# Performance work log

Hardware: AMD Instinct MI355X
Metric: run time of the kernel (lower is better)

Reference implementation:

```python
import jax, jax.numpy as jnp
import numpy as np

N_NODES = 262144
N_EDGES = 524288
EMB = 256
HID = 256
NODE_VOC = 50000
POS_VOC = 1000
LN_EPS = 1e-5


def layer_norm(x, g, b):
    m = jnp.mean(x, axis=-1, keepdims=True)
    v = jnp.var(x, axis=-1, keepdims=True)
    return (x - m) * jax.lax.rsqrt(v + LN_EPS) * g + b


def sage_conv(x, src, dst, Wl, bl, Wr):
    # PyG SAGEConv, aggr='add': out = lin_l(sum_{j in N(i)} x_j) + lin_r(x_i)
    agg = jax.ops.segment_sum(x[src], dst, num_segments=N_NODES)  # [N, d_in]
    return agg @ Wl.T + bl + x @ Wr.T


def setup_inputs() -> dict:
    key = jax.random.key(0)
    ks = jax.random.split(key, 16)
    s = 0.02
    node_emb = jax.random.randint(ks[0], (N_NODES,), 0, NODE_VOC)
    pos = jax.random.randint(ks[1], (N_NODES,), 0, POS_VOC)
    edge = jax.random.randint(ks[2], (2, N_EDGES), 0, N_NODES)
    node_tab = jax.random.normal(ks[3], (NODE_VOC, EMB), jnp.float32) * s
    pos_tab = jax.random.normal(ks[4], (POS_VOC, EMB), jnp.float32) * s
    pos_tab = pos_tab.at[0].set(0.0)  # padding_idx=0
    g_emb = jnp.ones((EMB,), jnp.float32)
    b_emb = jnp.zeros((EMB,), jnp.float32)
    Wl0 = jax.random.normal(ks[5], (HID, EMB), jnp.float32) * s
    bl0 = jnp.zeros((HID,), jnp.float32)
    Wr0 = jax.random.normal(ks[6], (HID, EMB), jnp.float32) * s
    g0 = jnp.ones((HID,), jnp.float32)
    b0 = jnp.zeros((HID,), jnp.float32)
    Wl1 = jax.random.normal(ks[7], (EMB, HID), jnp.float32) * s
    bl1 = jnp.zeros((EMB,), jnp.float32)
    Wr1 = jax.random.normal(ks[8], (EMB, HID), jnp.float32) * s
    g1 = jnp.ones((EMB,), jnp.float32)
    b1 = jnp.zeros((EMB,), jnp.float32)
    return {"node_emb": node_emb, "pos": pos, "edge": edge,
            "node_tab": node_tab, "pos_tab": pos_tab,
            "g_emb": g_emb, "b_emb": b_emb,
            "Wl0": Wl0, "bl0": bl0, "Wr0": Wr0, "g0": g0, "b0": b0,
            "Wl1": Wl1, "bl1": bl1, "Wr1": Wr1, "g1": g1, "b1": b1}


def reference(node_emb, pos, edge, node_tab, pos_tab, g_emb, b_emb,
              Wl0, bl0, Wr0, g0, b0, Wl1, bl1, Wr1, g1, b1):
    src, dst = edge[0], edge[1]
    # embed + scale + positional emb; dropout is identity in eval
    h = node_tab[node_emb] * jnp.sqrt(jnp.float32(EMB)) + pos_tab[pos]
    h = layer_norm(h, g_emb, b_emb)
    for (Wl, bl, Wr, g, b) in ((Wl0, bl0, Wr0, g0, b0), (Wl1, bl1, Wr1, g1, b1)):
        h_ = jax.nn.relu(sage_conv(h, src, dst, Wl, bl, Wr))
        h = layer_norm(h_ + h, g, b)
    return h
```

## Files before the change

### kernel.cpp

```cpp
#include <hip/hip_runtime.h>
#include <hip/hip_bf16.h>
#include <stdint.h>

#define N_NODES 262144
#define N_EDGES 524288
#define EMB 256
#define LN_EPS 1e-5f

typedef unsigned short u16;
typedef unsigned int u32;
typedef __bf16 bf16_t;
typedef __bf16 bf16x8 __attribute__((ext_vector_type(8)));
typedef float f32x4 __attribute__((ext_vector_type(4)));

__device__ __forceinline__ u16 f2bf(float f) {
    u32 u = __float_as_uint(f);
    u32 r = u + 0x7fffu + ((u >> 16) & 1u);
    return (u16)(r >> 16);
}
__device__ __forceinline__ float bf2f(u16 b) { return __uint_as_float(((u32)b) << 16); }
__device__ __forceinline__ float lo16(u32 x) { return __uint_as_float(x << 16); }
__device__ __forceinline__ float hi16(u32 x) { return __uint_as_float(x & 0xffff0000u); }

__device__ __forceinline__ void async_copy16(void* lds, const void* g) {
    __builtin_amdgcn_global_load_lds(
        (const __attribute__((address_space(1))) u32*)g,
        (__attribute__((address_space(3))) u32*)lds, 16, 0, 0);
}

__global__ __launch_bounds__(256) void convert_w_kernel(
    const float* __restrict__ a, const float* __restrict__ b,
    const float* __restrict__ c, const float* __restrict__ d,
    u16* __restrict__ out)
{
    int seg = blockIdx.x >> 6;
    int blk = blockIdx.x & 63;
    const float* src = (seg == 0) ? a : (seg == 1) ? b : (seg == 2) ? c : d;
    int off = blk * 1024 + threadIdx.x * 4;
    float4 v = *(const float4*)(src + off);
    uint2 o;
    o.x = (u32)f2bf(v.x) | ((u32)f2bf(v.y) << 16);
    o.y = (u32)f2bf(v.z) | ((u32)f2bf(v.w) << 16);
    *(uint2*)(out + seg * 65536 + off) = o;
}

__global__ __launch_bounds__(256) void embed_ln_kernel(
    const int* __restrict__ node_emb, const int* __restrict__ pos,
    const float* __restrict__ node_tab, const float* __restrict__ pos_tab,
    const float* __restrict__ g_emb, const float* __restrict__ b_emb,
    u16* __restrict__ h0)
{
    const int wid = threadIdx.x >> 6, lane = threadIdx.x & 63;
    const int row = blockIdx.x * 4 + wid;
    const int idx = node_emb[row];
    const int p = pos[row];
    float4 ra = *(const float4*)(node_tab + (size_t)idx * EMB + lane * 4);
    float4 rb = *(const float4*)(pos_tab + (size_t)p * EMB + lane * 4);
    float v0 = ra.x * 16.f + rb.x;
    float v1 = ra.y * 16.f + rb.y;
    float v2 = ra.z * 16.f + rb.z;
    float v3 = ra.w * 16.f + rb.w;
    float s = v0 + v1 + v2 + v3;
    float sq = v0 * v0 + v1 * v1 + v2 * v2 + v3 * v3;
    #pragma unroll
    for (int m = 1; m < 64; m <<= 1) { s += __shfl_xor(s, m); sq += __shfl_xor(sq, m); }
    float mean = s * (1.f / 256.f);
    float var = sq * (1.f / 256.f) - mean * mean;
    float rstd = rsqrtf(var + LN_EPS);
    float4 rg = *(const float4*)(g_emb + lane * 4);
    float4 rbt = *(const float4*)(b_emb + lane * 4);
    float o0 = (v0 - mean) * rstd * rg.x + rbt.x;
    float o1 = (v1 - mean) * rstd * rg.y + rbt.y;
    float o2 = (v2 - mean) * rstd * rg.z + rbt.z;
    float o3 = (v3 - mean) * rstd * rg.w + rbt.w;
    uint2 out;
    out.x = (u32)f2bf(o0) | ((u32)f2bf(o1) << 16);
    out.y = (u32)f2bf(o2) | ((u32)f2bf(o3) << 16);
    *(uint2*)(h0 + (size_t)row * EMB + lane * 4) = out;
}

__global__ __launch_bounds__(256) void hist_kernel(const int* __restrict__ dst, int* __restrict__ deg) {
    int e = blockIdx.x * 256 + threadIdx.x;
    atomicAdd(&deg[dst[e]], 1);
}

__global__ __launch_bounds__(1024) void scan1_kernel(const int* __restrict__ deg,
                                                     int* __restrict__ incl, int* __restrict__ bsum) {
    __shared__ int tmp[1024];
    int t = threadIdx.x, g = blockIdx.x * 1024 + t;
    tmp[t] = deg[g];
    __syncthreads();
    for (int off = 1; off < 1024; off <<= 1) {
        int x = (t >= off) ? tmp[t - off] : 0;
        __syncthreads();
        tmp[t] += x;
        __syncthreads();
    }
    incl[g] = tmp[t];
    if (t == 1023) bsum[blockIdx.x] = tmp[t];
}

__global__ __launch_bounds__(256) void scan2_kernel(const int* __restrict__ bsum, int* __restrict__ boff) {
    __shared__ int tmp[256];
    int t = threadIdx.x;
    int own = bsum[t];
    tmp[t] = own;
    __syncthreads();
    for (int off = 1; off < 256; off <<= 1) {
        int x = (t >= off) ? tmp[t - off] : 0;
        __syncthreads();
        tmp[t] += x;
        __syncthreads();
    }
    boff[t] = tmp[t] - own;
}

__global__ __launch_bounds__(256) void scan3_kernel(const int* __restrict__ incl, const int* __restrict__ deg,
                                                    const int* __restrict__ boff,
                                                    int* __restrict__ rowstart, int* __restrict__ cursor) {
    int g = blockIdx.x * 256 + threadIdx.x;
    int v = incl[g] - deg[g] + boff[g >> 10];
    rowstart[g] = v;
    cursor[g] = v;
    if (g == N_NODES - 1) rowstart[N_NODES] = N_EDGES;
}

__global__ __launch_bounds__(256) void scatter_kernel(const int* __restrict__ src, const int* __restrict__ dst,
                                                      int* __restrict__ cursor, int* __restrict__ csr) {
    int e = blockIdx.x * 256 + threadIdx.x;
    int slot = atomicAdd(&cursor[dst[e]], 1);
    csr[slot] = src[e];
}

template<bool F32OUT>
__global__ __launch_bounds__(512, 4) void gemm_fused_kernel(
    const u16* __restrict__ Hin,
    const int* __restrict__ rowstart, const int* __restrict__ csr,
    const u16* __restrict__ Wl, const u16* __restrict__ Wr,
    const float* __restrict__ bias, const float* __restrict__ gam, const float* __restrict__ bet,
    u16* __restrict__ outb, float* __restrict__ outf)
{
    __shared__ alignas(16) u16 aggA[4 * 64 * 64];
    __shared__ alignas(16) u16 lB[256 * 64];
    __shared__ float s_sum[64];
    __shared__ float s_sq[64];

    const int tid = threadIdx.x;
    const int wid = tid >> 6, lane = tid & 63;
    const int quad = lane >> 4, l16 = lane & 15;
    const int wrow = wid >> 2, wcol = wid & 3;
    const int m0 = blockIdx.x * 64;
    const int lsrc = ((lane & 7) ^ (lane >> 3)) * 8;

    auto stageB = [&](int s) {
        const int k0 = s * 64;
        const u16* Bsrc = (k0 < 256) ? (Wl + k0) : (Wr + (k0 - 256));
        #pragma unroll
        for (int t = 0; t < 4; ++t) {
            int q = wid * 4 + t;
            int n = q * 8 + (lane >> 3);
            async_copy16((char*)lB + q * 1024, Bsrc + (size_t)n * EMB + lsrc);
        }
    };
    auto stageH = [&](int t) {
        int row = tid >> 3;
        int kg = (tid & 7) ^ (row & 7);
        async_copy16((char*)aggA + (t - 4) * 8192 + tid * 16,
                     Hin + (size_t)(m0 + row) * EMB + (t - 4) * 64 + kg * 8);
    };

    stageB(0);

    {
        const int grp = tid >> 5, gl = tid & 31;
        #pragma unroll
        for (int i = 0; i < 4; ++i) {
            const int r = grp * 4 + i;
            const int node = m0 + r;
            const int beg = rowstart[node];
            const int end = rowstart[node + 1];
            float a0[8] = {}, a1[8] = {};
            int j = beg;
            for (; j + 1 < end; j += 2) {
                int s0 = csr[j], s1 = csr[j + 1];
                uint4 r0 = *(const uint4*)(Hin + (size_t)s0 * EMB + gl * 8);
                uint4 r1 = *(const uint4*)(Hin + (size_t)s1 * EMB + gl * 8);
                a0[0] += lo16(r0.x); a0[1] += hi16(r0.x);
                a0[2] += lo16(r0.y); a0[3] += hi16(r0.y);
                a0[4] += lo16(r0.z); a0[5] += hi16(r0.z);
                a0[6] += lo16(r0.w); a0[7] += hi16(r0.w);
                a1[0] += lo16(r1.x); a1[1] += hi16(r1.x);
                a1[2] += lo16(r1.y); a1[3] += hi16(r1.y);
                a1[4] += lo16(r1.z); a1[5] += hi16(r1.z);
                a1[6] += lo16(r1.w); a1[7] += hi16(r1.w);
            }
            if (j < end) {
                int s0 = csr[j];
                uint4 r0 = *(const uint4*)(Hin + (size_t)s0 * EMB + gl * 8);
                a0[0] += lo16(r0.x); a0[1] += hi16(r0.x);
                a0[2] += lo16(r0.y); a0[3] += hi16(r0.y);
                a0[4] += lo16(r0.z); a0[5] += hi16(r0.z);
                a0[6] += lo16(r0.w); a0[7] += hi16(r0.w);
            }
            uint4 o;
            o.x = (u32)f2bf(a0[0] + a1[0]) | ((u32)f2bf(a0[1] + a1[1]) << 16);
            o.y = (u32)f2bf(a0[2] + a1[2]) | ((u32)f2bf(a0[3] + a1[3]) << 16);
            o.z = (u32)f2bf(a0[4] + a1[4]) | ((u32)f2bf(a0[5] + a1[5]) << 16);
            o.w = (u32)f2bf(a0[6] + a1[6]) | ((u32)f2bf(a0[7] + a1[7]) << 16);
            int cg = (gl & 7) ^ (r & 7);
            *(uint4*)&aggA[(gl >> 3) * 4096 + r * 64 + cg * 8] = o;
        }
    }
    asm volatile("s_waitcnt lgkmcnt(0)\n\ts_barrier" ::: "memory");

    f32x4 acc[2][4] = {};
    #pragma unroll
    for (int s = 0; s < 8; ++s) {
        if (s > 0) stageB(s);
        if (s >= 1 && s <= 4) stageH(s + 3);
        if (s >= 1 && s <= 4) asm volatile("s_waitcnt vmcnt(1)\n\ts_barrier" ::: "memory");
        else                  asm volatile("s_waitcnt vmcnt(0)\n\ts_barrier" ::: "memory");

        const u16* la = aggA + (s & 3) * 4096;
        #pragma unroll
        for (int kk = 0; kk < 2; ++kk) {
            const int g = (((kk * 4 + quad) ^ (l16 & 7)) * 8);
            bf16x8 af[2], bfr[4];
            #pragma unroll
            for (int mt = 0; mt < 2; ++mt)
                af[mt] = *(const bf16x8*)&la[(wrow * 32 + mt * 16 + l16) * 64 + g];
            #pragma unroll
            for (int nt = 0; nt < 4; ++nt)
                bfr[nt] = *(const bf16x8*)&lB[(wcol * 64 + nt * 16 + l16) * 64 + g];
            #pragma unroll
            for (int mt = 0; mt < 2; ++mt)
                #pragma unroll
                for (int nt = 0; nt < 4; ++nt)
                    acc[mt][nt] = __builtin_amdgcn_mfma_f32_16x16x32_bf16(af[mt], bfr[nt], acc[mt][nt], 0, 0, 0);
        }
        asm volatile("s_waitcnt lgkmcnt(0)\n\ts_barrier" ::: "memory");
    }

    if (tid < 64) { s_sum[tid] = 0.f; s_sq[tid] = 0.f; }
    __syncthreads();

    const int cb = wcol * 64;
    float blv[4], gv[4], bv[4];
    #pragma unroll
    for (int nt = 0; nt < 4; ++nt) {
        int col = cb + nt * 16 + l16;
        blv[nt] = bias[col]; gv[nt] = gam[col]; bv[nt] = bet[col];
    }

    #pragma unroll
    for (int mt = 0; mt < 2; ++mt) {
        #pragma unroll
        for (int i = 0; i < 4; ++i) {
            int r = wrow * 32 + mt * 16 + quad * 4 + i;
            int rowg = m0 + r;
            float rs = 0.f, rq = 0.f;
            #pragma unroll
            for (int nt = 0; nt < 4; ++nt) {
                int col = cb + nt * 16 + l16;
                float v = acc[mt][nt][i] + blv[nt];
                v = fmaxf(v, 0.f);
                v += bf2f(Hin[(size_t)rowg * EMB + col]);
                acc[mt][nt][i] = v;
                rs += v; rq += v * v;
            }
            #pragma unroll
            for (int m = 1; m < 16; m <<= 1) { rs += __shfl_xor(rs, m); rq += __shfl_xor(rq, m); }
            if (l16 == 0) { atomicAdd(&s_sum[r], rs); atomicAdd(&s_sq[r], rq); }
        }
    }
    __syncthreads();

    #pragma unroll
    for (int mt = 0; mt < 2; ++mt) {
        #pragma unroll
        for (int i = 0; i < 4; ++i) {
            int r = wrow * 32 + mt * 16 + quad * 4 + i;
            int rowg = m0 + r;
            float mean = s_sum[r] * (1.f / 256.f);
            float var = s_sq[r] * (1.f / 256.f) - mean * mean;
            float rstd = rsqrtf(var + LN_EPS);
            #pragma unroll
            for (int nt = 0; nt < 4; ++nt) {
                int col = cb + nt * 16 + l16;
                float o = (acc[mt][nt][i] - mean) * rstd * gv[nt] + bv[nt];
                if (F32OUT) outf[(size_t)rowg * EMB + col] = o;
                else        outb[(size_t)rowg * EMB + col] = f2bf(o);
            }
        }
    }
}

extern "C" void kernel_launch(void* const* d_in, const int* in_sizes, int n_in,
                              void* d_out, int out_size, void* d_ws, size_t ws_size,
                              hipStream_t stream)
{
    const int* node_emb = (const int*)d_in[0];
    const int* pos      = (const int*)d_in[1];
    const int* edge     = (const int*)d_in[2];
    const float* node_tab = (const float*)d_in[3];
    const float* pos_tab  = (const float*)d_in[4];
    const float* g_emb    = (const float*)d_in[5];
    const float* b_emb    = (const float*)d_in[6];
    const float* Wl0 = (const float*)d_in[7];
    const float* bl0 = (const float*)d_in[8];
    const float* Wr0 = (const float*)d_in[9];
    const float* g0  = (const float*)d_in[10];
    const float* b0  = (const float*)d_in[11];
    const float* Wl1 = (const float*)d_in[12];
    const float* bl1 = (const float*)d_in[13];
    const float* Wr1 = (const float*)d_in[14];
    const float* g1  = (const float*)d_in[15];
    const float* b1  = (const float*)d_in[16];

    char* w = (char*)d_ws;
    auto alloc = [&](size_t bytes) { char* p = w; w += (bytes + 255) & ~(size_t)255; return p; };
    u16* h0       = (u16*)alloc((size_t)N_NODES * EMB * 2);
    u16* h1       = (u16*)alloc((size_t)N_NODES * EMB * 2);
    u16* wbf      = (u16*)alloc((size_t)4 * 65536 * 2);
    int* deg      = (int*)alloc((size_t)N_NODES * 4);
    int* incl     = (int*)alloc((size_t)N_NODES * 4);
    int* rowstart = (int*)alloc((size_t)(N_NODES + 1) * 4);
    int* cursor   = (int*)alloc((size_t)N_NODES * 4);
    int* csr      = (int*)alloc((size_t)N_EDGES * 4);
    int* bsum     = (int*)alloc(256 * 4);
    int* boff     = (int*)alloc(256 * 4);

    float* outf = (float*)d_out;

    const int* srcv = edge;
    const int* dstv = edge + N_EDGES;

    hipMemsetAsync(deg, 0, (size_t)N_NODES * 4, stream);
    convert_w_kernel<<<256, 256, 0, stream>>>(Wl0, Wr0, Wl1, Wr1, wbf);
    embed_ln_kernel<<<N_NODES / 4, 256, 0, stream>>>(node_emb, pos, node_tab, pos_tab, g_emb, b_emb, h0);
    hist_kernel<<<N_EDGES / 256, 256, 0, stream>>>(dstv, deg);
    scan1_kernel<<<N_NODES / 1024, 1024, 0, stream>>>(deg, incl, bsum);
    scan2_kernel<<<1, 256, 0, stream>>>(bsum, boff);
    scan3_kernel<<<N_NODES / 256, 256, 0, stream>>>(incl, deg, boff, rowstart, cursor);
    scatter_kernel<<<N_EDGES / 256, 256, 0, stream>>>(srcv, dstv, cursor, csr);

    gemm_fused_kernel<false><<<N_NODES / 64, 512, 0, stream>>>(
        h0, rowstart, csr, wbf, wbf + 65536, bl0, g0, b0, h1, nullptr);
    gemm_fused_kernel<true><<<N_NODES / 64, 512, 0, stream>>>(
        h1, rowstart, csr, wbf + 131072, wbf + 196608, bl1, g1, b1, nullptr, outf);
}
```

Baseline: 855.7 us.

## Stage CSR indices in LDS and widen per-thread gather to 32 bytes

Before aggregation, the block's 64 rowstart entries and up to 1024 CSR neighbor indices are preloaded into shared memory, so the gather loop reads indices from LDS instead of issuing dependent global loads. Each thread now handles 16 features (two 16-byte loads per neighbor) across 2 rows instead of 8 features across 4 rows, which doubles the loads in flight per thread. The row loop is no longer unrolled. The costs are an extra barrier, about 4 KB more LDS (which may affect occupancy at launch_bounds(512,4)), and higher register pressure from 32 accumulators.

```diff
diff --git a/kernel.cpp b/kernel.cpp
--- a/kernel.cpp
+++ b/kernel.cpp
@@ -6,6 +6,7 @@
 #define N_EDGES 524288
 #define EMB 256
 #define LN_EPS 1e-5f
+#define CSR_CAP 1024
 
 typedef unsigned short u16;
 typedef unsigned int u32;
@@ -142,6 +143,8 @@
 {
     __shared__ alignas(16) u16 aggA[4 * 64 * 64];
     __shared__ alignas(16) u16 lB[256 * 64];
+    __shared__ int ls_row[72];
+    __shared__ int lcsr[CSR_CAP];
     __shared__ float s_sum[64];
     __shared__ float s_sq[64];
 
@@ -171,44 +174,77 @@
 
     stageB(0);
 
+    const int beg_all = rowstart[m0];
+    const int end_all = rowstart[m0 + 64];
+    const int cnt = end_all - beg_all;
+    if (tid < 65) ls_row[tid] = rowstart[m0 + tid];
+    const int lim = (cnt < CSR_CAP) ? cnt : CSR_CAP;
+    for (int e = tid; e < lim; e += 512) lcsr[e] = csr[beg_all + e];
+    asm volatile("s_waitcnt lgkmcnt(0)\n\ts_barrier" ::: "memory");
+
     {
-        const int grp = tid >> 5, gl = tid & 31;
-        #pragma unroll
-        for (int i = 0; i < 4; ++i) {
-            const int r = grp * 4 + i;
-            const int node = m0 + r;
-            const int beg = rowstart[node];
-            const int end = rowstart[node + 1];
-            float a0[8] = {}, a1[8] = {};
+        const int grp = tid >> 4, gl = tid & 15;
+        #pragma unroll 1
+        for (int i = 0; i < 2; ++i) {
+            const int r = grp * 2 + i;
+            const int beg = ls_row[r];
+            const int end = ls_row[r + 1];
+            float a0[16] = {}, a1[16] = {};
             int j = beg;
             for (; j + 1 < end; j += 2) {
-                int s0 = csr[j], s1 = csr[j + 1];
-                uint4 r0 = *(const uint4*)(Hin + (size_t)s0 * EMB + gl * 8);
-                uint4 r1 = *(const uint4*)(Hin + (size_t)s1 * EMB + gl * 8);
-                a0[0] += lo16(r0.x); a0[1] += hi16(r0.x);
-                a0[2] += lo16(r0.y); a0[3] += hi16(r0.y);
-                a0[4] += lo16(r0.z); a0[5] += hi16(r0.z);
-                a0[6] += lo16(r0.w); a0[7] += hi16(r0.w);
-                a1[0] += lo16(r1.x); a1[1] += hi16(r1.x);
-                a1[2] += lo16(r1.y); a1[3] += hi16(r1.y);
-                a1[4] += lo16(r1.z); a1[5] += hi16(r1.z);
-                a1[6] += lo16(r1.w); a1[7] += hi16(r1.w);
+                int sl0 = j - beg_all, sl1 = sl0 + 1;
+                int s0 = (sl0 < CSR_CAP) ? lcsr[sl0] : csr[j];
+                int s1 = (sl1 < CSR_CAP) ? lcsr[sl1] : csr[j + 1];
+                const u16* p0 = Hin + (size_t)s0 * EMB + gl * 16;
+                const u16* p1 = Hin + (size_t)s1 * EMB + gl * 16;
+                uint4 q0 = *(const uint4*)p0, q2 = *(const uint4*)(p0 + 8);
+                uint4 q1 = *(const uint4*)p1, q3 = *(const uint4*)(p1 + 8);
+                a0[0]  += lo16(q0.x); a0[1]  += hi16(q0.x);
+                a0[2]  += lo16(q0.y); a0[3]  += hi16(q0.y);
+                a0[4]  += lo16(q0.z); a0[5]  += hi16(q0.z);
+                a0[6]  += lo16(q0.w); a0[7]  += hi16(q0.w);
+                a0[8]  += lo16(q2.x); a0[9]  += hi16(q2.x);
+                a0[10] += lo16(q2.y); a0[11] += hi16(q2.y);
+                a0[12] += lo16(q2.z); a0[13] += hi16(q2.z);
+                a0[14] += lo16(q2.w); a0[15] += hi16(q2.w);
+                a1[0]  += lo16(q1.x); a1[1]  += hi16(q1.x);
+                a1[2]  += lo16(q1.y); a1[3]  += hi16(q1.y);
+                a1[4]  += lo16(q1.z); a1[5]  += hi16(q1.z);
+                a1[6]  += lo16(q1.w); a1[7]  += hi16(q1.w);
+                a1[8]  += lo16(q3.x); a1[9]  += hi16(q3.x);
+                a1[10] += lo16(q3.y); a1[11] += hi16(q3.y);
+                a1[12] += lo16(q3.z); a1[13] += hi16(q3.z);
+                a1[14] += lo16(q3.w); a1[15] += hi16(q3.w);
             }
             if (j < end) {
-                int s0 = csr[j];
-                uint4 r0 = *(const uint4*)(Hin + (size_t)s0 * EMB + gl * 8);
-                a0[0] += lo16(r0.x); a0[1] += hi16(r0.x);
-                a0[2] += lo16(r0.y); a0[3] += hi16(r0.y);
-                a0[4] += lo16(r0.z); a0[5] += hi16(r0.z);
-                a0[6] += lo16(r0.w); a0[7] += hi16(r0.w);
+                int sl0 = j - beg_all;
+                int s0 = (sl0 < CSR_CAP) ? lcsr[sl0] : csr[j];
+                const u16* p0 = Hin + (size_t)s0 * EMB + gl * 16;
+                uint4 q0 = *(const uint4*)p0, q2 = *(const uint4*)(p0 + 8);
+                a0[0]  += lo16(q0.x); a0[1]  += hi16(q0.x);
+                a0[2]  += lo16(q0.y); a0[3]  += hi16(q0.y);
+                a0[4]  += lo16(q0.z); a0[5]  += hi16(q0.z);
+                a0[6]  += lo16(q0.w); a0[7]  += hi16(q0.w);
+                a0[8]  += lo16(q2.x); a0[9]  += hi16(q2.x);
+                a0[10] += lo16(q2.y); a0[11] += hi16(q2.y);
+                a0[12] += lo16(q2.z); a0[13] += hi16(q2.z);
+                a0[14] += lo16(q2.w); a0[15] += hi16(q2.w);
             }
-            uint4 o;
-            o.x = (u32)f2bf(a0[0] + a1[0]) | ((u32)f2bf(a0[1] + a1[1]) << 16);
-            o.y = (u32)f2bf(a0[2] + a1[2]) | ((u32)f2bf(a0[3] + a1[3]) << 16);
-            o.z = (u32)f2bf(a0[4] + a1[4]) | ((u32)f2bf(a0[5] + a1[5]) << 16);
-            o.w = (u32)f2bf(a0[6] + a1[6]) | ((u32)f2bf(a0[7] + a1[7]) << 16);
-            int cg = (gl & 7) ^ (r & 7);
-            *(uint4*)&aggA[(gl >> 3) * 4096 + r * 64 + cg * 8] = o;
+            uint4 o0, o1;
+            o0.x = (u32)f2bf(a0[0]  + a1[0])  | ((u32)f2bf(a0[1]  + a1[1])  << 16);
+            o0.y = (u32)f2bf(a0[2]  + a1[2])  | ((u32)f2bf(a0[3]  + a1[3])  << 16);
+            o0.z = (u32)f2bf(a0[4]  + a1[4])  | ((u32)f2bf(a0[5]  + a1[5])  << 16);
+            o0.w = (u32)f2bf(a0[6]  + a1[6])  | ((u32)f2bf(a0[7]  + a1[7])  << 16);
+            o1.x = (u32)f2bf(a0[8]  + a1[8])  | ((u32)f2bf(a0[9]  + a1[9])  << 16);
+            o1.y = (u32)f2bf(a0[10] + a1[10]) | ((u32)f2bf(a0[11] + a1[11]) << 16);
+            o1.z = (u32)f2bf(a0[12] + a1[12]) | ((u32)f2bf(a0[13] + a1[13]) << 16);
+            o1.w = (u32)f2bf(a0[14] + a1[14]) | ((u32)f2bf(a0[15] + a1[15]) << 16);
+            int kg0 = (2 * gl) & 7;
+            int cg0 = kg0 ^ (r & 7);
+            int cg1 = (kg0 + 1) ^ (r & 7);
+            u16* base = &aggA[(gl >> 2) * 4096 + r * 64];
+            *(uint4*)(base + cg0 * 8) = o0;
+            *(uint4*)(base + cg1 * 8) = o1;
         }
     }
     asm volatile("s_waitcnt lgkmcnt(0)\n\ts_barrier" ::: "memory");
```

Measured after the change: 810.2 us. -5.3%, faster.

## Stage block CSR in LDS, gather two rows per group, reuse staged H for residual

Applied to the files above, without the earlier changes.

The block's CSR neighbor indices and row starts are preloaded into shared memory up to a fixed cap, with a global fallback beyond it. The gather is restructured so each 16-lane group processes two rows at once with 32-byte loads per lane, raising memory-level parallelism. The residual term in the epilogue is now read from the H tile already staged in LDS instead of being reloaded from global memory. The costs are more registers from the larger accumulators, which may reduce occupancy, and an extra barrier before the gather.

```diff
diff --git a/kernel.cpp b/kernel.cpp
--- a/kernel.cpp
+++ b/kernel.cpp
@@ -6,6 +6,7 @@
 #define N_EDGES 524288
 #define EMB 256
 #define LN_EPS 1e-5f
+#define CSR_CAP 1024
 
 typedef unsigned short u16;
 typedef unsigned int u32;
@@ -142,6 +143,8 @@
 {
     __shared__ alignas(16) u16 aggA[4 * 64 * 64];
     __shared__ alignas(16) u16 lB[256 * 64];
+    __shared__ int ls_row[72];
+    __shared__ int lcsr[CSR_CAP];
     __shared__ float s_sum[64];
     __shared__ float s_sq[64];
 
@@ -171,44 +174,140 @@
 
     stageB(0);
 
+    const int beg_all = rowstart[m0];
+    const int end_all = rowstart[m0 + 64];
+    const int cnt = end_all - beg_all;
+    if (tid < 65) ls_row[tid] = rowstart[m0 + tid];
+    const int lim = (cnt < CSR_CAP) ? cnt : CSR_CAP;
+    for (int e = tid; e < lim; e += 512) lcsr[e] = csr[beg_all + e];
+    asm volatile("s_waitcnt lgkmcnt(0)\n\ts_barrier" ::: "memory");
+
     {
-        const int grp = tid >> 5, gl = tid & 31;
-        #pragma unroll
-        for (int i = 0; i < 4; ++i) {
-            const int r = grp * 4 + i;
-            const int node = m0 + r;
-            const int beg = rowstart[node];
-            const int end = rowstart[node + 1];
-            float a0[8] = {}, a1[8] = {};
-            int j = beg;
-            for (; j + 1 < end; j += 2) {
-                int s0 = csr[j], s1 = csr[j + 1];
-                uint4 r0 = *(const uint4*)(Hin + (size_t)s0 * EMB + gl * 8);
-                uint4 r1 = *(const uint4*)(Hin + (size_t)s1 * EMB + gl * 8);
-                a0[0] += lo16(r0.x); a0[1] += hi16(r0.x);
-                a0[2] += lo16(r0.y); a0[3] += hi16(r0.y);
-                a0[4] += lo16(r0.z); a0[5] += hi16(r0.z);
-                a0[6] += lo16(r0.w); a0[7] += hi16(r0.w);
-                a1[0] += lo16(r1.x); a1[1] += hi16(r1.x);
-                a1[2] += lo16(r1.y); a1[3] += hi16(r1.y);
-                a1[4] += lo16(r1.z); a1[5] += hi16(r1.z);
-                a1[6] += lo16(r1.w); a1[7] += hi16(r1.w);
-            }
-            if (j < end) {
-                int s0 = csr[j];
-                uint4 r0 = *(const uint4*)(Hin + (size_t)s0 * EMB + gl * 8);
-                a0[0] += lo16(r0.x); a0[1] += hi16(r0.x);
-                a0[2] += lo16(r0.y); a0[3] += hi16(r0.y);
-                a0[4] += lo16(r0.z); a0[5] += hi16(r0.z);
-                a0[6] += lo16(r0.w); a0[7] += hi16(r0.w);
-            }
-            uint4 o;
-            o.x = (u32)f2bf(a0[0] + a1[0]) | ((u32)f2bf(a0[1] + a1[1]) << 16);
-            o.y = (u32)f2bf(a0[2] + a1[2]) | ((u32)f2bf(a0[3] + a1[3]) << 16);
-            o.z = (u32)f2bf(a0[4] + a1[4]) | ((u32)f2bf(a0[5] + a1[5]) << 16);
-            o.w = (u32)f2bf(a0[6] + a1[6]) | ((u32)f2bf(a0[7] + a1[7]) << 16);
-            int cg = (gl & 7) ^ (r & 7);
-            *(uint4*)&aggA[(gl >> 3) * 4096 + r * 64 + cg * 8] = o;
+        const int grp = tid >> 4, gl = tid & 15;
+        const int r0 = grp * 2, r1 = r0 + 1;
+        const int begr0 = ls_row[r0];
+        const int endr0 = ls_row[r0 + 1];
+        const int endr1 = ls_row[r1 + 1];
+        float A0[16] = {}, A1[16] = {};
+        float B0[16] = {}, B1[16] = {};
+        int j0 = begr0, j1 = endr0;
+        while ((j0 + 1 < endr0) | (j1 + 1 < endr1)) {
+            bool v0 = (j0 + 1 < endr0), v1 = (j1 + 1 < endr1);
+            int s00, s01, s10, s11;
+            uint4 q0, q1, q2, q3, p0, p1, p2, p3;
+            if (v0) {
+                int sl = j0 - beg_all;
+                s00 = (sl < CSR_CAP) ? lcsr[sl] : csr[j0];
+                s01 = (sl + 1 < CSR_CAP) ? lcsr[sl + 1] : csr[j0 + 1];
+                const u16* pa = Hin + (size_t)s00 * EMB + gl * 16;
+                const u16* pb = Hin + (size_t)s01 * EMB + gl * 16;
+                q0 = *(const uint4*)pa; q2 = *(const uint4*)(pa + 8);
+                q1 = *(const uint4*)pb; q3 = *(const uint4*)(pb + 8);
+            }
+            if (v1) {
+                int sl = j1 - beg_all;
+                s10 = (sl < CSR_CAP) ? lcsr[sl] : csr[j1];
+                s11 = (sl + 1 < CSR_CAP) ? lcsr[sl + 1] : csr[j1 + 1];
+                const u16* pa = Hin + (size_t)s10 * EMB + gl * 16;
+                const u16* pb = Hin + (size_t)s11 * EMB + gl * 16;
+                p0 = *(const uint4*)pa; p2 = *(const uint4*)(pa + 8);
+                p1 = *(const uint4*)pb; p3 = *(const uint4*)(pb + 8);
+            }
+            if (v0) {
+                A0[0]  += lo16(q0.x); A0[1]  += hi16(q0.x);
+                A0[2]  += lo16(q0.y); A0[3]  += hi16(q0.y);
+                A0[4]  += lo16(q0.z); A0[5]  += hi16(q0.z);
+                A0[6]  += lo16(q0.w); A0[7]  += hi16(q0.w);
+                A0[8]  += lo16(q2.x); A0[9]  += hi16(q2.x);
+                A0[10] += lo16(q2.y); A0[11] += hi16(q2.y);
+                A0[12] += lo16(q2.z); A0[13] += hi16(q2.z);
+                A0[14] += lo16(q2.w); A0[15] += hi16(q2.w);
+                A1[0]  += lo16(q1.x); A1[1]  += hi16(q1.x);
+                A1[2]  += lo16(q1.y); A1[3]  += hi16(q1.y);
+                A1[4]  += lo16(q1.z); A1[5]  += hi16(q1.z);
+                A1[6]  += lo16(q1.w); A1[7]  += hi16(q1.w);
+                A1[8]  += lo16(q3.x); A1[9]  += hi16(q3.x);
+                A1[10] += lo16(q3.y); A1[11] += hi16(q3.y);
+                A1[12] += lo16(q3.z); A1[13] += hi16(q3.z);
+                A1[14] += lo16(q3.w); A1[15] += hi16(q3.w);
+                j0 += 2;
+            }
+            if (v1) {
+                B0[0]  += lo16(p0.x); B0[1]  += hi16(p0.x);
+                B0[2]  += lo16(p0.y); B0[3]  += hi16(p0.y);
+                B0[4]  += lo16(p0.z); B0[5]  += hi16(p0.z);
+                B0[6]  += lo16(p0.w); B0[7]  += hi16(p0.w);
+                B0[8]  += lo16(p2.x); B0[9]  += hi16(p2.x);
+                B0[10] += lo16(p2.y); B0[11] += hi16(p2.y);
+                B0[12] += lo16(p2.z); B0[13] += hi16(p2.z);
+                B0[14] += lo16(p2.w); B0[15] += hi16(p2.w);
+                B1[0]  += lo16(p1.x); B1[1]  += hi16(p1.x);
+                B1[2]  += lo16(p1.y); B1[3]  += hi16(p1.y);
+                B1[4]  += lo16(p1.z); B1[5]  += hi16(p1.z);
+                B1[6]  += lo16(p1.w); B1[7]  += hi16(p1.w);
+                B1[8]  += lo16(p3.x); B1[9]  += hi16(p3.x);
+                B1[10] += lo16(p3.y); B1[11] += hi16(p3.y);
+                B1[12] += lo16(p3.z); B1[13] += hi16(p3.z);
+                B1[14] += lo16(p3.w); B1[15] += hi16(p3.w);
+                j1 += 2;
+            }
+        }
+        if (j0 < endr0) {
+            int sl = j0 - beg_all;
+            int s0 = (sl < CSR_CAP) ? lcsr[sl] : csr[j0];
+            const u16* pa = Hin + (size_t)s0 * EMB + gl * 16;
+            uint4 q0 = *(const uint4*)pa, q2 = *(const uint4*)(pa + 8);
+            A0[0]  += lo16(q0.x); A0[1]  += hi16(q0.x);
+            A0[2]  += lo16(q0.y); A0[3]  += hi16(q0.y);
+            A0[4]  += lo16(q0.z); A0[5]  += hi16(q0.z);
+            A0[6]  += lo16(q0.w); A0[7]  += hi16(q0.w);
+            A0[8]  += lo16(q2.x); A0[9]  += hi16(q2.x);
+            A0[10] += lo16(q2.y); A0[11] += hi16(q2.y);
+            A0[12] += lo16(q2.z); A0[13] += hi16(q2.z);
+            A0[14] += lo16(q2.w); A0[15] += hi16(q2.w);
+        }
+        if (j1 < endr1) {
+            int sl = j1 - beg_all;
+            int s0 = (sl < CSR_CAP) ? lcsr[sl] : csr[j1];
+            const u16* pa = Hin + (size_t)s0 * EMB + gl * 16;
+            uint4 p0 = *(const uint4*)pa, p2 = *(const uint4*)(pa + 8);
+            B0[0]  += lo16(p0.x); B0[1]  += hi16(p0.x);
+            B0[2]  += lo16(p0.y); B0[3]  += hi16(p0.y);
+            B0[4]  += lo16(p0.z); B0[5]  += hi16(p0.z);
+            B0[6]  += lo16(p0.w); B0[7]  += hi16(p0.w);
+            B0[8]  += lo16(p2.x); B0[9]  += hi16(p2.x);
+            B0[10] += lo16(p2.y); B0[11] += hi16(p2.y);
+            B0[12] += lo16(p2.z); B0[13] += hi16(p2.z);
+            B0[14] += lo16(p2.w); B0[15] += hi16(p2.w);
+        }
+        const int kg0 = (2 * gl) & 7;
+        {
+            uint4 o0, o1;
+            o0.x = (u32)f2bf(A0[0]  + A1[0])  | ((u32)f2bf(A0[1]  + A1[1])  << 16);
+            o0.y = (u32)f2bf(A0[2]  + A1[2])  | ((u32)f2bf(A0[3]  + A1[3])  << 16);
+            o0.z = (u32)f2bf(A0[4]  + A1[4])  | ((u32)f2bf(A0[5]  + A1[5])  << 16);
+            o0.w = (u32)f2bf(A0[6]  + A1[6])  | ((u32)f2bf(A0[7]  + A1[7])  << 16);
+            o1.x = (u32)f2bf(A0[8]  + A1[8])  | ((u32)f2bf(A0[9]  + A1[9])  << 16);
+            o1.y = (u32)f2bf(A0[10] + A1[10]) | ((u32)f2bf(A0[11] + A1[11]) << 16);
+            o1.z = (u32)f2bf(A0[12] + A1[12]) | ((u32)f2bf(A0[13] + A1[13]) << 16);
+            o1.w = (u32)f2bf(A0[14] + A1[14]) | ((u32)f2bf(A0[15] + A1[15]) << 16);
+            u16* base = &aggA[(gl >> 2) * 4096 + r0 * 64];
+            *(uint4*)(base + (kg0 ^ (r0 & 7)) * 8) = o0;
+            *(uint4*)(base + ((kg0 + 1) ^ (r0 & 7)) * 8) = o1;
+        }
+        {
+            uint4 o0, o1;
+            o0.x = (u32)f2bf(B0[0]  + B1[0])  | ((u32)f2bf(B0[1]  + B1[1])  << 16);
+            o0.y = (u32)f2bf(B0[2]  + B1[2])  | ((u32)f2bf(B0[3]  + B1[3])  << 16);
+            o0.z = (u32)f2bf(B0[4]  + B1[4])  | ((u32)f2bf(B0[5]  + B1[5])  << 16);
+            o0.w = (u32)f2bf(B0[6]  + B1[6])  | ((u32)f2bf(B0[7]  + B1[7])  << 16);
+            o1.x = (u32)f2bf(B0[8]  + B1[8])  | ((u32)f2bf(B0[9]  + B1[9])  << 16);
+            o1.y = (u32)f2bf(B0[10] + B1[10]) | ((u32)f2bf(B0[11] + B1[11]) << 16);
+            o1.z = (u32)f2bf(B0[12] + B1[12]) | ((u32)f2bf(B0[13] + B1[13]) << 16);
+            o1.w = (u32)f2bf(B0[14] + B1[14]) | ((u32)f2bf(B0[15] + B1[15]) << 16);
+            u16* base = &aggA[(gl >> 2) * 4096 + r1 * 64];
+            *(uint4*)(base + (kg0 ^ (r1 & 7)) * 8) = o0;
+            *(uint4*)(base + ((kg0 + 1) ^ (r1 & 7)) * 8) = o1;
         }
     }
     asm volatile("s_waitcnt lgkmcnt(0)\n\ts_barrier" ::: "memory");
@@ -257,14 +356,14 @@
         #pragma unroll
         for (int i = 0; i < 4; ++i) {
             int r = wrow * 32 + mt * 16 + quad * 4 + i;
-            int rowg = m0 + r;
             float rs = 0.f, rq = 0.f;
             #pragma unroll
             for (int nt = 0; nt < 4; ++nt) {
-                int col = cb + nt * 16 + l16;
+                int c = nt * 16 + l16;
+                float res = bf2f(aggA[wcol * 4096 + r * 64 + (((c >> 3) ^ (r & 7)) << 3) + (c & 7)]);
                 float v = acc[mt][nt][i] + blv[nt];
                 v = fmaxf(v, 0.f);
-                v += bf2f(Hin[(size_t)rowg * EMB + col]);
+                v += res;
                 acc[mt][nt][i] = v;
                 rs += v; rq += v * v;
             }
```

After: 820.3 us. 1.04x faster.
